# Optimization experiments

Measured on AMD Instinct MI355X. Metric: run time of the kernel, lower is better.

## Reference

```python
import jax, jax.numpy as jnp
import numpy as np

B, N, E = 16, 50000, 1600000  # batch, num_nodes (excl. ground), num_edges


def setup_inputs() -> dict:
    key = jax.random.key(0)
    k1, k2, k3, k4 = jax.random.split(key, 4)
    x = jax.random.normal(k1, (B, N), dtype=jnp.float32)
    # node indices in [0, N]; index 0 is the ground node prepended in forward
    src_node = jax.random.randint(k2, (E,), 0, N + 1)
    des_node = jax.random.randint(k3, (E,), 0, N + 1)
    # per-edge device params (a, w, b), gauss init std=0.01 per _init_model_param
    param = jax.random.normal(k4, (3, E), dtype=jnp.float32) * 0.01
    t = jnp.zeros((1,), dtype=jnp.float32)
    return {"t": t, "x": x, "param": param, "src_node": src_node, "des_node": des_node}


def _edge_model(param, v_s, v_d):
    # per-edge nonlinear device current: i_e = a_e * tanh(w_e*(v_s - v_d) + b_e)
    a, w, b = param[0], param[1], param[2]
    return a * jnp.tanh(w * (v_s - v_d) + b)  # (B, E)


def reference(t, x, param, src_node, des_node):
    # prepend ground node (voltage 0) -> aux_v: (B, N+1)
    aux_v = jnp.concatenate([jnp.zeros_like(x[..., :1]), x], axis=-1)
    v_s = aux_v[:, src_node]  # gather (B, E)
    v_d = aux_v[:, des_node]  # gather (B, E)
    state_i = _edge_model(param, v_s, v_d)  # (B, E)
    # KCL: current leaves src, enters des; scatter_add along node axis
    res = jnp.zeros_like(aux_v)
    res = res.at[:, src_node].add(-state_i)
    res = res.at[:, des_node].add(state_i)
    return res[:, 1:]  # drop ground node
```

## Files before the change

### kernel.cpp

```cpp
#include <hip/hip_runtime.h>

#define BATCH 16
#define PS 49
#define NPART 1024
#define SB 256
#define TPB 1024
#define LDSCAP 3840

static __device__ __forceinline__ float fast_tanh(float z) {
    float ez = __expf(2.0f * z);
    return 1.0f - 2.0f * __builtin_amdgcn_rcpf(ez + 1.0f);
}

__global__ void build_aux_T(const float* __restrict__ x, float* __restrict__ auxT, int n) {
    int idx = blockIdx.x * blockDim.x + threadIdx.x;
    if (idx >= BATCH * n) return;
    int b = idx / n;
    int i = idx % n;
    auxT[(i + 1) * BATCH + b] = x[idx];
    if (idx < BATCH) auxT[idx] = 0.0f;
}

__global__ __launch_bounds__(TPB)
void hist1(const int* __restrict__ src, const int* __restrict__ des,
           unsigned* __restrict__ blockHist, int E) {
    __shared__ unsigned h[NPART];
    int tid = threadIdx.x;
    for (int i = tid; i < NPART; i += TPB) h[i] = 0;
    __syncthreads();
    long t = (long)blockIdx.x * TPB + tid;
    long stride = (long)gridDim.x * TPB * 4;
    for (long e0 = t * 4; e0 < E; e0 += stride) {
        int ne = (int)min((long)4, (long)E - e0);
        int ss[4], dd[4];
        if (ne == 4) {
            int4 sv = *(const int4*)(src + e0);
            int4 dv = *(const int4*)(des + e0);
            ss[0]=sv.x; ss[1]=sv.y; ss[2]=sv.z; ss[3]=sv.w;
            dd[0]=dv.x; dd[1]=dv.y; dd[2]=dv.z; dd[3]=dv.w;
        } else {
            for (int j = 0; j < ne; ++j) { ss[j] = src[e0+j]; dd[j] = des[e0+j]; }
        }
        for (int j = 0; j < ne; ++j) {
            atomicAdd(&h[ss[j] / PS], 1u);
            atomicAdd(&h[dd[j] / PS], 1u);
        }
    }
    __syncthreads();
    for (int i = tid; i < NPART; i += TPB)
        blockHist[(size_t)blockIdx.x * NPART + i] = h[i];
}

__global__ __launch_bounds__(TPB)
void scan1(unsigned* __restrict__ blockHist, unsigned* __restrict__ partStart) {
    __shared__ unsigned bst[NPART + 1];
    int tid = threadIdx.x;
    unsigned sum = 0;
    for (int r = 0; r < SB; ++r) sum += blockHist[(size_t)r * NPART + tid];
    bst[tid] = sum;
    __syncthreads();
    if (tid == 0) {
        unsigned run = 0;
        for (int i = 0; i < NPART; ++i) { unsigned t = bst[i]; bst[i] = run; run += t; }
        bst[NPART] = run;
    }
    __syncthreads();
    partStart[tid] = bst[tid];
    if (tid == 0) partStart[NPART] = bst[NPART];
    unsigned run = bst[tid];
    for (int r = 0; r < SB; ++r) {
        unsigned tmp = blockHist[(size_t)r * NPART + tid];
        blockHist[(size_t)r * NPART + tid] = run;
        run += tmp;
    }
}

__global__ __launch_bounds__(TPB)
void scatter1(const int* __restrict__ src, const int* __restrict__ des,
              const float* __restrict__ param, const unsigned* __restrict__ offsets,
              uint4* __restrict__ bins, int E) {
    __shared__ unsigned offs[NPART];
    int tid = threadIdx.x;
    for (int i = tid; i < NPART; i += TPB)
        offs[i] = offsets[(size_t)blockIdx.x * NPART + i];
    __syncthreads();
    long t = (long)blockIdx.x * TPB + tid;
    long stride = (long)gridDim.x * TPB * 4;
    for (long e0 = t * 4; e0 < E; e0 += stride) {
        int ne = (int)min((long)4, (long)E - e0);
        int ss[4], dd[4];
        float aa[4], ww[4], cc[4];
        if (ne == 4) {
            int4 sv = *(const int4*)(src + e0);
            int4 dv = *(const int4*)(des + e0);
            float4 av = *(const float4*)(param + e0);
            float4 wv = *(const float4*)(param + E + e0);
            float4 cv = *(const float4*)(param + 2 * (size_t)E + e0);
            ss[0]=sv.x; ss[1]=sv.y; ss[2]=sv.z; ss[3]=sv.w;
            dd[0]=dv.x; dd[1]=dv.y; dd[2]=dv.z; dd[3]=dv.w;
            aa[0]=av.x; aa[1]=av.y; aa[2]=av.z; aa[3]=av.w;
            ww[0]=wv.x; ww[1]=wv.y; ww[2]=wv.z; ww[3]=wv.w;
            cc[0]=cv.x; cc[1]=cv.y; cc[2]=cv.z; cc[3]=cv.w;
        } else {
            for (int j = 0; j < ne; ++j) {
                ss[j] = src[e0+j]; dd[j] = des[e0+j];
                aa[j] = param[e0+j]; ww[j] = param[E + e0 + j];
                cc[j] = param[2 * (size_t)E + e0 + j];
            }
        }
        for (int j = 0; j < ne; ++j) {
            int s = ss[j], d = dd[j];
            unsigned slot = atomicAdd(&offs[s / PS], 1u);
            bins[slot] = make_uint4((unsigned)s | ((unsigned)d << 16),
                                    __float_as_uint(-aa[j]), __float_as_uint(ww[j]),
                                    __float_as_uint(cc[j]));
            unsigned slot2 = atomicAdd(&offs[d / PS], 1u);
            bins[slot2] = make_uint4((unsigned)d | ((unsigned)s << 16),
                                     __float_as_uint(aa[j]), __float_as_uint(-ww[j]),
                                     __float_as_uint(cc[j]));
        }
    }
}

__global__ __launch_bounds__(TPB)
void sort_accumulate(const uint4* __restrict__ bins, const unsigned* __restrict__ partStart,
                     const float* __restrict__ auxT, float* __restrict__ outT, int n) {
    extern __shared__ uint4 srec[];
    unsigned* bump = (unsigned*)(srec + LDSCAP);
    unsigned* ns   = bump + PS;
    int p = blockIdx.x;
    int tid = threadIdx.x;
    unsigned lo = partStart[p], hi = partStart[p + 1];
    unsigned cnt = hi - lo;
    unsigned cl = cnt < (unsigned)LDSCAP ? cnt : (unsigned)LDSCAP;
    int base = p * PS;

    for (int i = tid; i < PS; i += TPB) bump[i] = 0;
    __syncthreads();
    const unsigned* keys = (const unsigned*)bins;
    for (unsigned k = tid; k < cl; k += TPB) {
        unsigned o = keys[(size_t)(lo + k) * 4] & 0xFFFFu;
        atomicAdd(&bump[o - (unsigned)base], 1u);
    }
    __syncthreads();
    if (tid == 0) {
        unsigned run = 0;
        for (int i = 0; i < PS; ++i) {
            unsigned c = bump[i];
            ns[i] = run;
            bump[i] = run;
            run += c;
        }
        ns[PS] = run;
    }
    __syncthreads();
    for (unsigned k = tid; k < cl; k += TPB) {
        uint4 rec = bins[lo + k];
        unsigned slot = atomicAdd(&bump[(rec.x & 0xFFFFu) - (unsigned)base], 1u);
        srec[slot] = rec;
    }
    __syncthreads();
    int lane = tid & 63;
    int wv = tid >> 6;
    int ri = lane >> 2, lj = lane & 3;
    const float4* aux4 = (const float4*)auxT;
    float4* out4 = (float4*)outT;
    for (int nl = wv; nl < PS; nl += TPB / 64) {
        int node = base + nl;
        if (node == 0 || node > n) continue;
        unsigned l2 = ns[nl], h2 = ns[nl + 1];
        float4 vo = aux4[(size_t)node * 4 + lj];
        float ax = 0.0f, ay = 0.0f, az = 0.0f, as_ = 0.0f;
        for (unsigned kk = l2; kk < h2; kk += 16) {
            unsigned k = kk + (unsigned)ri;
            uint4 rec;
            if (k < h2) rec = srec[k];
            else { rec.x = 0u; rec.y = 0u; rec.z = 0u; rec.w = 0u; }
            unsigned rem = rec.x >> 16;
            float4 vr = aux4[(size_t)rem * 4 + lj];
            float a = __uint_as_float(rec.y);
            float w = __uint_as_float(rec.z);
            float c = __uint_as_float(rec.w);
            ax  += a * fast_tanh(w * (vo.x - vr.x) + c);
            ay  += a * fast_tanh(w * (vo.y - vr.y) + c);
            az  += a * fast_tanh(w * (vo.z - vr.z) + c);
            as_ += a * fast_tanh(w * (vo.w - vr.w) + c);
        }
        for (unsigned kk = lo + cl; kk < hi; kk += 16) {
            unsigned k = kk + (unsigned)ri;
            uint4 rec;
            if (k < hi) rec = bins[k];
            else { rec.x = 0u; rec.y = 0u; rec.z = 0u; rec.w = 0u; }
            if ((int)(rec.x & 0xFFFFu) != node) rec.y = 0u;
            unsigned rem = rec.x >> 16;
            float4 vr = aux4[(size_t)rem * 4 + lj];
            float a = __uint_as_float(rec.y);
            float w = __uint_as_float(rec.z);
            float c = __uint_as_float(rec.w);
            ax  += a * fast_tanh(w * (vo.x - vr.x) + c);
            ay  += a * fast_tanh(w * (vo.y - vr.y) + c);
            az  += a * fast_tanh(w * (vo.z - vr.z) + c);
            as_ += a * fast_tanh(w * (vo.w - vr.w) + c);
        }
#pragma unroll
        for (int m = 4; m < 64; m <<= 1) {
            ax  += __shfl_xor(ax, m, 64);
            ay  += __shfl_xor(ay, m, 64);
            az  += __shfl_xor(az, m, 64);
            as_ += __shfl_xor(as_, m, 64);
        }
        if (lane < 4)
            out4[(size_t)node * 4 + lane] = make_float4(ax, ay, az, as_);
    }
}

__global__ void transpose_out(const float* __restrict__ outT, float* __restrict__ out, int n) {
    int idx = blockIdx.x * blockDim.x + threadIdx.x;
    if (idx >= BATCH * n) return;
    int b = idx / n;
    int j = idx % n;
    out[idx] = outT[(size_t)(j + 1) * BATCH + b];
}

__global__ void edge_direct(const float* __restrict__ param,
                            const int* __restrict__ src,
                            const int* __restrict__ des,
                            const float* __restrict__ x,
                            float* __restrict__ out, int E, int n) {
    int e = blockIdx.x * blockDim.x + threadIdx.x;
    if (e >= E) return;
    float a = param[e], w = param[E + e], c = param[2 * E + e];
    int s = src[e], d = des[e];
#pragma unroll
    for (int b = 0; b < BATCH; ++b) {
        float vs = s ? x[(size_t)b * n + (s - 1)] : 0.0f;
        float vd = d ? x[(size_t)b * n + (d - 1)] : 0.0f;
        float st = a * tanhf(w * (vs - vd) + c);
        if (s) atomicAdd(out + (size_t)b * n + (s - 1), -st);
        if (d) atomicAdd(out + (size_t)b * n + (d - 1), st);
    }
}

extern "C" void kernel_launch(void* const* d_in, const int* in_sizes, int n_in,
                              void* d_out, int out_size, void* d_ws, size_t ws_size,
                              hipStream_t stream) {
    const float* x     = (const float*)d_in[1];
    const float* param = (const float*)d_in[2];
    const int*   src   = (const int*)d_in[3];
    const int*   des   = (const int*)d_in[4];
    float* out = (float*)d_out;

    int E = in_sizes[3];
    int n = in_sizes[1] / BATCH;
    int total = BATCH * n;

    auto alignup = [](size_t v) { return (v + 255) & ~(size_t)255; };
    size_t auxBytes  = alignup((size_t)(n + 1) * BATCH * sizeof(float));
    size_t outTBytes = auxBytes;
    size_t bhBytes   = alignup((size_t)SB * NPART * sizeof(unsigned));
    size_t psBytes   = alignup((size_t)(NPART + 1) * sizeof(unsigned));
    size_t binBytes  = alignup((size_t)2 * E * sizeof(uint4));
    size_t need      = auxBytes + outTBytes + bhBytes + psBytes + binBytes;

    size_t saLds = (size_t)LDSCAP * sizeof(uint4) + (2 * PS + 1 + 8) * sizeof(unsigned);

    if (ws_size >= need && (n + 1) <= NPART * PS && n <= 65534) {
        char* w = (char*)d_ws;
        float*    auxT      = (float*)w;     w += auxBytes;
        float*    outT      = (float*)w;     w += outTBytes;
        unsigned* blockHist = (unsigned*)w;  w += bhBytes;
        unsigned* partStart = (unsigned*)w;  w += psBytes;
        uint4*    bins      = (uint4*)w;

        build_aux_T<<<(total + 255) / 256, 256, 0, stream>>>(x, auxT, n);
        hist1<<<SB, TPB, 0, stream>>>(src, des, blockHist, E);
        scan1<<<1, TPB, 0, stream>>>(blockHist, partStart);
        scatter1<<<SB, TPB, 0, stream>>>(src, des, param, blockHist, bins, E);
        sort_accumulate<<<NPART, TPB, saLds, stream>>>(bins, partStart, auxT, outT, n);
        transpose_out<<<(total + 255) / 256, 256, 0, stream>>>(outT, out, n);
        return;
    }

    (void)hipMemsetAsync(out, 0, (size_t)out_size * sizeof(float), stream);
    edge_direct<<<(E + 255) / 256, 256, 0, stream>>>(param, src, des, x, out, E, n);
}
```

Measured before the change: 134.0 us.

## Parallelize bin-offset scan across multiple blocks with wave-level shuffles

Replaces the single-block scan1 kernel, which had each thread walk 256 rows serially and used a serial 1024-element scan on thread 0, with three kernels. A 16-block kernel computes per-bin totals using 16 lanes per bin, a single-block kernel scans them with wave shuffles, and a 16-block kernel writes per-block offsets from a segmented shuffle prefix. The goal is to remove the serial latency of the old scan. The cost is two extra kernel launches and a second read of the histogram.

```diff
diff --git a/kernel.cpp b/kernel.cpp
--- a/kernel.cpp
+++ b/kernel.cpp
@@ -52,25 +52,64 @@
 }
 
 __global__ __launch_bounds__(TPB)
-void scan1(unsigned* __restrict__ blockHist, unsigned* __restrict__ partStart) {
-    __shared__ unsigned bst[NPART + 1];
-    int tid = threadIdx.x;
-    unsigned sum = 0;
-    for (int r = 0; r < SB; ++r) sum += blockHist[(size_t)r * NPART + tid];
-    bst[tid] = sum;
-    __syncthreads();
-    if (tid == 0) {
-        unsigned run = 0;
-        for (int i = 0; i < NPART; ++i) { unsigned t = bst[i]; bst[i] = run; run += t; }
-        bst[NPART] = run;
-    }
-    __syncthreads();
-    partStart[tid] = bst[tid];
-    if (tid == 0) partStart[NPART] = bst[NPART];
-    unsigned run = bst[tid];
-    for (int r = 0; r < SB; ++r) {
-        unsigned tmp = blockHist[(size_t)r * NPART + tid];
-        blockHist[(size_t)r * NPART + tid] = run;
+void totals_k(const unsigned* __restrict__ blockHist, unsigned* __restrict__ binTotal) {
+    int tid = threadIdx.x;
+    int bin = blockIdx.x * 64 + (tid >> 4);
+    int j = tid & 15;
+    unsigned s = 0;
+    for (int r = j; r < SB; r += 16) s += blockHist[(size_t)r * NPART + bin];
+#pragma unroll
+    for (int m = 1; m < 16; m <<= 1) s += __shfl_xor(s, m, 64);
+    if (j == 0) binTotal[bin] = s;
+}
+
+__global__ __launch_bounds__(TPB)
+void scan_bins(const unsigned* __restrict__ binTotal, unsigned* __restrict__ partStart) {
+    __shared__ unsigned wsum[16];
+    int tid = threadIdx.x;
+    int lane = tid & 63, wv = tid >> 6;
+    unsigned v = binTotal[tid];
+    unsigned inc = v;
+    for (int off = 1; off < 64; off <<= 1) {
+        unsigned t = __shfl_up(inc, off, 64);
+        if (lane >= off) inc += t;
+    }
+    if (lane == 63) wsum[wv] = inc;
+    __syncthreads();
+    if (tid < 16) {
+        unsigned w = wsum[tid], winc = w;
+        for (int off = 1; off < 16; off <<= 1) {
+            unsigned t = __shfl_up(winc, off, 64);
+            if (tid >= off) winc += t;
+        }
+        wsum[tid] = winc - w;
+    }
+    __syncthreads();
+    unsigned excl = (inc - v) + wsum[wv];
+    partStart[tid] = excl;
+    if (tid == TPB - 1) partStart[NPART] = excl + v;
+}
+
+__global__ __launch_bounds__(TPB)
+void offs_k(unsigned* __restrict__ blockHist, const unsigned* __restrict__ partStart) {
+    int tid = threadIdx.x;
+    int binLocal = tid >> 4;
+    int bin = blockIdx.x * 64 + binLocal;
+    int j = tid & 15;
+    const int per = SB / 16;
+    unsigned ls = 0;
+    for (int r = j * per; r < (j + 1) * per; ++r)
+        ls += blockHist[(size_t)r * NPART + bin];
+    int waveBase = (binLocal & 3) * 16;
+    unsigned excl = 0;
+    for (int k = 0; k < 16; ++k) {
+        unsigned v = __shfl(ls, waveBase + k, 64);
+        if (k < j) excl += v;
+    }
+    unsigned run = partStart[bin] + excl;
+    for (int r = j * per; r < (j + 1) * per; ++r) {
+        unsigned tmp = blockHist[(size_t)r * NPART + bin];
+        blockHist[(size_t)r * NPART + bin] = run;
         run += tmp;
     }
 }
@@ -259,8 +298,9 @@
     size_t outTBytes = auxBytes;
     size_t bhBytes   = alignup((size_t)SB * NPART * sizeof(unsigned));
     size_t psBytes   = alignup((size_t)(NPART + 1) * sizeof(unsigned));
+    size_t btBytes   = alignup((size_t)NPART * sizeof(unsigned));
     size_t binBytes  = alignup((size_t)2 * E * sizeof(uint4));
-    size_t need      = auxBytes + outTBytes + bhBytes + psBytes + binBytes;
+    size_t need      = auxBytes + outTBytes + bhBytes + psBytes + btBytes + binBytes;
 
     size_t saLds = (size_t)LDSCAP * sizeof(uint4) + (2 * PS + 1 + 8) * sizeof(unsigned);
 
@@ -270,11 +310,14 @@
         float*    outT      = (float*)w;     w += outTBytes;
         unsigned* blockHist = (unsigned*)w;  w += bhBytes;
         unsigned* partStart = (unsigned*)w;  w += psBytes;
+        unsigned* binTotal  = (unsigned*)w;  w += btBytes;
         uint4*    bins      = (uint4*)w;
 
         build_aux_T<<<(total + 255) / 256, 256, 0, stream>>>(x, auxT, n);
         hist1<<<SB, TPB, 0, stream>>>(src, des, blockHist, E);
-        scan1<<<1, TPB, 0, stream>>>(blockHist, partStart);
+        totals_k<<<NPART / 64, TPB, 0, stream>>>(blockHist, binTotal);
+        scan_bins<<<1, TPB, 0, stream>>>(binTotal, partStart);
+        offs_k<<<NPART / 64, TPB, 0, stream>>>(blockHist, partStart);
         scatter1<<<SB, TPB, 0, stream>>>(src, des, param, blockHist, bins, E);
         sort_accumulate<<<NPART, TPB, saLds, stream>>>(bins, partStart, auxT, outT, n);
         transpose_out<<<(total + 255) / 256, 256, 0, stream>>>(outT, out, n);
```

After: 127.1 us. 1.05x faster.
